# Performance work log

Measured on AMD Instinct MI355X. Metric: run time of the kernel, lower is better.

## Reference

```python
import jax, jax.numpy as jnp
import numpy as np

B, L, D, H, HID = 2048, 512, 17, 8, 256  # batch, max entities, feat dim, heads, mlp hidden
SPECIAL, OUT = 9, 23  # special vector dims, policy logits (7+16)


def _lin(k, out_d, in_d, scale):
    kw, kb = jax.random.split(k)
    W = jax.random.normal(kw, (out_d, in_d), jnp.float32) * scale
    b = jax.random.normal(kb, (out_d,), jnp.float32) * 0.01
    return W, b


def setup_inputs() -> dict:
    key = jax.random.key(0)
    ks = jax.random.split(key, 16)
    # observations: row 0 holds the 9-dim special vector, rows 1..L are ragged entities
    x = jax.random.normal(ks[0], (B, L + 1, D), jnp.float32)
    lengths = jax.random.randint(ks[1], (B,), 1, L + 1)
    mask = (jnp.arange(L)[None, :] < lengths[:, None]).astype(jnp.float32)
    x = x.at[:, 1:, :].multiply(mask[:, :, None])  # zero rows mark padding
    s = 1.0 / np.sqrt(D)
    # per-head K/V projections (num_heads separate tiny Linears)
    Wk = jax.random.normal(ks[2], (H, D, D), jnp.float32) * s
    bk = jax.random.normal(ks[3], (H, D), jnp.float32) * 0.01
    Wv = jax.random.normal(ks[4], (H, D, D), jnp.float32) * s
    bv = jax.random.normal(ks[5], (H, D), jnp.float32) * 0.01
    q = jax.random.normal(ks[6], (H, D), jnp.float32)  # learned per-head queries
    Wo, bo = _lin(ks[7], D, H * D, 1.0 / np.sqrt(H * D))
    sc = 1.0 / np.sqrt(D + SPECIAL)
    pW1, pb1 = _lin(ks[8], HID, D + SPECIAL, sc)
    pW2, pb2 = _lin(ks[9], HID, HID, 1.0 / np.sqrt(HID))
    pW3, pb3 = _lin(ks[10], OUT, HID, 1.0 / np.sqrt(HID))
    vW1, vb1 = _lin(ks[11], HID, D + SPECIAL, sc)
    vW2, vb2 = _lin(ks[12], HID, HID, 1.0 / np.sqrt(HID))
    vW3, vb3 = _lin(ks[13], 1, HID, 1.0 / np.sqrt(HID))
    return dict(x=x, Wk=Wk, bk=bk, Wv=Wv, bv=bv, q=q, Wo=Wo, bo=bo,
                pW1=pW1, pb1=pb1, pW2=pW2, pb2=pb2, pW3=pW3, pb3=pb3,
                vW1=vW1, vb1=vb1, vW2=vW2, vb2=vb2, vW3=vW3, vb3=vb3)


def _mlp(h, W1, b1, W2, b2, W3, b3):
    h = jax.nn.relu(h @ W1.T + b1)
    h = jax.nn.relu(h @ W2.T + b2)
    return h @ W3.T + b3


def reference(x, Wk, bk, Wv, bv, q, Wo, bo,
              pW1, pb1, pW2, pb2, pW3, pb3,
              vW1, vb1, vW2, vb2, vW3, vb3):
    special = x[:, 0, :SPECIAL]            # [B, 9]
    seq = x[:, 1:, :]                      # [B, L, D]
    mask = jnp.sum(jnp.abs(seq), axis=-1) != 0  # [B, L] non-padded rows
    # per-head keys/values for all samples at once (batched over the head loop)
    keys = jnp.einsum('bld,hed->bhle', seq, Wk) + bk[None, :, None, :]   # [B,H,L,D]
    vals = jnp.einsum('bld,hed->bhle', seq, Wv) + bv[None, :, None, :]   # [B,H,L,D]
    scores = jnp.einsum('bhle,he->bhl', keys, q)                          # [B,H,L]
    scores = jnp.where(mask[:, None, :], scores, -1e9)
    w = jax.nn.softmax(scores, axis=-1)                                   # [B,H,L]
    agg = jnp.einsum('bhl,bhle->bhe', w, vals).reshape(x.shape[0], H * D)  # concat heads
    attn = agg @ Wo.T + bo                                                # [B, D]
    comb = jnp.concatenate([attn, special], axis=-1)                      # [B, D+9]
    logits = _mlp(comb, pW1, pb1, pW2, pb2, pW3, pb3)                     # [B, 23]
    value = _mlp(comb, vW1, vb1, vW2, vb2, vW3, vb3)                      # [B, 1]
    return logits, value
```

## Files before the change

### kernel.cpp

```cpp
#include <hip/hip_runtime.h>
#include <hip/hip_bf16.h>

#define B_ 2048
#define D_ 17
#define H_ 8
#define HID_ 256
#define OUT_ 23
#define XROW 8721
#define SEQN 8704
#define ROWP 20
#define LAST4 4465151

__device__ __forceinline__ float bclane(float v, int l) {
  return __uint_as_float(__builtin_amdgcn_readlane(__float_as_uint(v), l));
}

__global__ __launch_bounds__(256) void prep_kernel(
    const float* __restrict__ pW2, const float* __restrict__ vW2,
    const float* __restrict__ Wk, const float* __restrict__ bk,
    const float* __restrict__ q,
    float* __restrict__ pW2t, float* __restrict__ vW2t, float* __restrict__ qkc)
{
  const int bid = blockIdx.x;
  const int t = threadIdx.x;
  if (bid == 128) {
    if (t < H_ * D_) {
      const int h = t / D_, dd = t - h * D_;
      float s = 0.f;
      #pragma unroll
      for (int e = 0; e < D_; ++e) s = fmaf(Wk[h*289 + e*D_ + dd], q[h*D_ + e], s);
      qkc[h*18 + dd] = s;
    } else if (t < H_ * D_ + H_) {
      const int h = t - H_ * D_;
      float s = 0.f;
      #pragma unroll
      for (int e = 0; e < D_; ++e) s = fmaf(bk[h*D_ + e], q[h*D_ + e], s);
      qkc[h*18 + 17] = s;
    }
    return;
  }
  __shared__ float tile[32][33];
  const int m = bid >> 6, tid = bid & 63;
  const int ti = (tid >> 3) * 32, tk = (tid & 7) * 32;
  const float* src = m ? vW2 : pW2;
  float* dst = m ? vW2t : pW2t;
  const int tx = t & 31, ty = t >> 5;
  #pragma unroll
  for (int r = 0; r < 4; ++r) tile[ty + 8*r][tx] = src[(ti + ty + 8*r)*HID_ + tk + tx];
  __syncthreads();
  #pragma unroll
  for (int r = 0; r < 4; ++r) dst[(tk + ty + 8*r)*HID_ + ti + tx] = tile[tx][ty + 8*r];
}

__device__ __forceinline__ void stw(float* s_seq, int off, float val) {
  if ((unsigned)off < (unsigned)SEQN) {
    const int r = off / 17;
    const int c = off - r * 17;
    s_seq[r * ROWP + c] = val;
  }
}
__device__ __forceinline__ void stw4(float* s_seq, int off, float4 v) {
  stw(s_seq, off,     v.x);
  stw(s_seq, off + 1, v.y);
  stw(s_seq, off + 2, v.z);
  stw(s_seq, off + 3, v.w);
}

__global__ __launch_bounds__(256, 3) void attn_comb_kernel(
    const float* __restrict__ x, const float* __restrict__ qkc,
    const float* __restrict__ Wv, const float* __restrict__ bv,
    const float* __restrict__ Wo, const float* __restrict__ bo,
    float* __restrict__ comb)
{
  __shared__ __align__(16) float s_seq[512 * ROWP];
  __shared__ float s_part[4][H_][18];
  __shared__ float s_swn[136];
  __shared__ float s_agg[136];
  __shared__ float s_wp[136];

  const int t = threadIdx.x;
  const int b = blockIdx.x;
  const int w = t >> 6, lane = t & 63;
  const int hp = lane >> 4;
  const int rg = lane & 15;
  const int seq0 = b * XROW + D_;
  const int s4 = seq0 >> 2;
  const int phase = seq0 & 3;
  const float4* __restrict__ x4 = (const float4*)x;

  const float pv = x[seq0 + lane * 136];

  float4 s0, s1, s2, s3, sR4, s5, s6, s7, s8;
  s0  = x4[s4 + t];
  s1  = x4[s4 +  256 + t];
  s2  = x4[s4 +  512 + t];
  s3  = x4[s4 +  768 + t];
  sR4 = x4[s4 + 1024 + t];

  const unsigned long long live = __ballot(pv != 0.f) | 1ull;
  const int nrows = 8 * (64 - __builtin_clzll(live));
  const int rounds = min(9, (nrows * D_ + phase + 1023) >> 10);

  if (rounds > 5) s5 = x4[s4 + 1280 + t];
  if (rounds > 6) s6 = x4[s4 + 1536 + t];
  if (rounds > 7) s7 = x4[s4 + 1792 + t];
  int idx8 = s4 + 2048 + t; if (idx8 > LAST4) idx8 = LAST4;
  if (rounds > 8) s8 = x4[idx8];

  const float* q0 = qkc + (2*hp) * 18;
  float qk0[D_], qk1[D_];
  #pragma unroll
  for (int d = 0; d < D_; ++d) { qk0[d] = q0[d]; qk1[d] = q0[18 + d]; }
  const float ch0 = q0[17], ch1 = q0[35];

  {
    const int o0 = 4*t - phase;
    stw4(s_seq, o0,        s0);
    stw4(s_seq, o0 + 1024, s1);
    stw4(s_seq, o0 + 2048, s2);
    stw4(s_seq, o0 + 3072, s3);
    stw4(s_seq, o0 + 4096, sR4);
    if (rounds > 5) stw4(s_seq, o0 + 5120, s5);
    if (rounds > 6) stw4(s_seq, o0 + 6144, s6);
    if (rounds > 7) stw4(s_seq, o0 + 7168, s7);
    if (rounds > 8) stw4(s_seq, 4*idx8 - seq0, s8);
  }
  __syncthreads();

  float den0 = 0.f, den1 = 0.f;
  float acc0[D_], acc1[D_];
  #pragma unroll
  for (int d = 0; d < D_; ++d) { acc0[d] = 0.f; acc1[d] = 0.f; }

  auto dorow = [&](int row) {
    const bool ok = row < nrows;
    const float* rp = &s_seq[(ok ? row : 0) * ROWP];
    const float4 v0 = *(const float4*)rp;
    const float4 v1 = *(const float4*)(rp + 4);
    const float4 v2 = *(const float4*)(rp + 8);
    const float4 v3 = *(const float4*)(rp + 12);
    const float4 v4 = *(const float4*)(rp + 16);
    float sA = ch0, sB = ch1;
    sA = fmaf(qk0[0],  v0.x, sA); sB = fmaf(qk1[0],  v0.x, sB);
    sA = fmaf(qk0[1],  v0.y, sA); sB = fmaf(qk1[1],  v0.y, sB);
    sA = fmaf(qk0[2],  v0.z, sA); sB = fmaf(qk1[2],  v0.z, sB);
    sA = fmaf(qk0[3],  v0.w, sA); sB = fmaf(qk1[3],  v0.w, sB);
    sA = fmaf(qk0[4],  v1.x, sA); sB = fmaf(qk1[4],  v1.x, sB);
    sA = fmaf(qk0[5],  v1.y, sA); sB = fmaf(qk1[5],  v1.y, sB);
    sA = fmaf(qk0[6],  v1.z, sA); sB = fmaf(qk1[6],  v1.z, sB);
    sA = fmaf(qk0[7],  v1.w, sA); sB = fmaf(qk1[7],  v1.w, sB);
    sA = fmaf(qk0[8],  v2.x, sA); sB = fmaf(qk1[8],  v2.x, sB);
    sA = fmaf(qk0[9],  v2.y, sA); sB = fmaf(qk1[9],  v2.y, sB);
    sA = fmaf(qk0[10], v2.z, sA); sB = fmaf(qk1[10], v2.z, sB);
    sA = fmaf(qk0[11], v2.w, sA); sB = fmaf(qk1[11], v2.w, sB);
    sA = fmaf(qk0[12], v3.x, sA); sB = fmaf(qk1[12], v3.x, sB);
    sA = fmaf(qk0[13], v3.y, sA); sB = fmaf(qk1[13], v3.y, sB);
    sA = fmaf(qk0[14], v3.z, sA); sB = fmaf(qk1[14], v3.z, sB);
    sA = fmaf(qk0[15], v3.w, sA); sB = fmaf(qk1[15], v3.w, sB);
    sA = fmaf(qk0[16], v4.x, sA); sB = fmaf(qk1[16], v4.x, sB);
    const bool lv = ok && (v0.x != 0.f);
    const float p0 = lv ? __expf(sA) : 0.f;
    const float p1 = lv ? __expf(sB) : 0.f;
    den0 += p0; den1 += p1;
    acc0[0]  = fmaf(p0, v0.x, acc0[0]);  acc1[0]  = fmaf(p1, v0.x, acc1[0]);
    acc0[1]  = fmaf(p0, v0.y, acc0[1]);  acc1[1]  = fmaf(p1, v0.y, acc1[1]);
    acc0[2]  = fmaf(p0, v0.z, acc0[2]);  acc1[2]  = fmaf(p1, v0.z, acc1[2]);
    acc0[3]  = fmaf(p0, v0.w, acc0[3]);  acc1[3]  = fmaf(p1, v0.w, acc1[3]);
    acc0[4]  = fmaf(p0, v1.x, acc0[4]);  acc1[4]  = fmaf(p1, v1.x, acc1[4]);
    acc0[5]  = fmaf(p0, v1.y, acc0[5]);  acc1[5]  = fmaf(p1, v1.y, acc1[5]);
    acc0[6]  = fmaf(p0, v1.z, acc0[6]);  acc1[6]  = fmaf(p1, v1.z, acc1[6]);
    acc0[7]  = fmaf(p0, v1.w, acc0[7]);  acc1[7]  = fmaf(p1, v1.w, acc1[7]);
    acc0[8]  = fmaf(p0, v2.x, acc0[8]);  acc1[8]  = fmaf(p1, v2.x, acc1[8]);
    acc0[9]  = fmaf(p0, v2.y, acc0[9]);  acc1[9]  = fmaf(p1, v2.y, acc1[9]);
    acc0[10] = fmaf(p0, v2.z, acc0[10]); acc1[10] = fmaf(p1, v2.z, acc1[10]);
    acc0[11] = fmaf(p0, v2.w, acc0[11]); acc1[11] = fmaf(p1, v2.w, acc1[11]);
    acc0[12] = fmaf(p0, v3.x, acc0[12]); acc1[12] = fmaf(p1, v3.x, acc1[12]);
    acc0[13] = fmaf(p0, v3.y, acc0[13]); acc1[13] = fmaf(p1, v3.y, acc1[13]);
    acc0[14] = fmaf(p0, v3.z, acc0[14]); acc1[14] = fmaf(p1, v3.z, acc1[14]);
    acc0[15] = fmaf(p0, v3.w, acc0[15]); acc1[15] = fmaf(p1, v3.w, acc1[15]);
    acc0[16] = fmaf(p0, v4.x, acc0[16]); acc1[16] = fmaf(p1, v4.x, acc1[16]);
  };

  {
    const int s0r = w * 64;
    if (s0r < nrows) {
      dorow(s0r + rg);
      dorow(s0r + rg + 16);
      dorow(s0r + rg + 32);
      dorow(s0r + rg + 48);
    }
    const int s1r = 256 + w * 64;
    if (s1r < nrows) {
      dorow(s1r + rg);
      dorow(s1r + rg + 16);
      dorow(s1r + rg + 32);
      dorow(s1r + rg + 48);
    }
  }

  #pragma unroll
  for (int m = 1; m <= 8; m <<= 1) {
    den0 += __shfl_xor(den0, m, 64);
    den1 += __shfl_xor(den1, m, 64);
    #pragma unroll
    for (int d = 0; d < D_; ++d) {
      acc0[d] += __shfl_xor(acc0[d], m, 64);
      acc1[d] += __shfl_xor(acc1[d], m, 64);
    }
  }
  if (rg == 0) {
    float* p0p = &s_part[w][2*hp][0];
    float* p1p = &s_part[w][2*hp + 1][0];
    p0p[0] = den0; p1p[0] = den1;
    #pragma unroll
    for (int d = 0; d < D_; ++d) { p0p[1 + d] = acc0[d]; p1p[1 + d] = acc1[d]; }
  }
  __syncthreads();

  if (t < 136) {
    const int hh = t / D_, d = t - hh * D_;
    float dn = 0.f, ac = 0.f;
    #pragma unroll
    for (int ww = 0; ww < 4; ++ww) { dn += s_part[ww][hh][0]; ac += s_part[ww][hh][1 + d]; }
    s_swn[t] = ac / dn;
  }
  __syncthreads();
  if (t < 136) {
    const int hh = t / D_, e = t - hh * D_;
    float s = bv[t];
    #pragma unroll
    for (int d = 0; d < D_; ++d) s = fmaf(Wv[hh*289 + e*D_ + d], s_swn[hh*D_ + d], s);
    s_agg[t] = s;
  }
  __syncthreads();
  if (t < 136) {
    const int o = t >> 3, pt = t & 7;
    float s = 0.f;
    #pragma unroll
    for (int j = 0; j < D_; ++j) s = fmaf(Wo[o*136 + pt*D_ + j], s_agg[pt*D_ + j], s);
    s_wp[t] = s;
  }
  __syncthreads();
  if (t < D_) {
    float s = bo[t];
    #pragma unroll
    for (int pt = 0; pt < 8; ++pt) s += s_wp[t*8 + pt];
    comb[b*26 + t] = s;
  } else if (t < 26) {
    comb[b*26 + t] = x[b * XROW + (t - D_)];
  }
}

__global__ __launch_bounds__(512) void mlp_kernel(
    const float* __restrict__ comb,
    const float* __restrict__ pW1, const float* __restrict__ pb1,
    const float* __restrict__ pW2t, const float* __restrict__ pb2,
    const float* __restrict__ pW3, const float* __restrict__ pb3,
    const float* __restrict__ vW1, const float* __restrict__ vb1,
    const float* __restrict__ vW2t, const float* __restrict__ vb2,
    const float* __restrict__ vW3, const float* __restrict__ vb3,
    float* __restrict__ out)
{
  __shared__ float s_comb[8][26];
  __shared__ __align__(16) float s_red[2][3][8][HID_];
  __shared__ __align__(16) float s_h2[2][8][HID_];

  const int t = threadIdx.x;
  const int b0 = blockIdx.x * 8;
  const int p = t >> 8;
  const int kq = (t >> 6) & 3;
  const int ln = t & 63;

  if (t < 208) { const int bb = t / 26, k = t - bb*26; s_comb[bb][k] = comb[(size_t)(b0 + bb)*26 + k]; }
  __syncthreads();

  const float* W1  = p ? vW1  : pW1;   const float* B1 = p ? vb1 : pb1;
  const float* W2t = p ? vW2t : pW2t;  const float* B2 = p ? vb2 : pb2;

  float h[8];
  {
    const int i = kq * 64 + ln;
    float a[8];
    #pragma unroll
    for (int bb = 0; bb < 8; ++bb) a[bb] = 0.f;
    const float* wr = W1 + i * 26;
    for (int k = 0; k < 26; ++k) {
      const float wk = wr[k];
      #pragma unroll
      for (int bb = 0; bb < 8; ++bb) a[bb] = fmaf(wk, s_comb[bb][k], a[bb]);
    }
    const float bias = B1[i];
    #pragma unroll
    for (int bb = 0; bb < 8; ++bb) h[bb] = fmaxf(a[bb] + bias, 0.f);
  }

  float4 acc[8];
  #pragma unroll
  for (int bb = 0; bb < 8; ++bb) acc[bb] = make_float4(0.f, 0.f, 0.f, 0.f);
  {
    const float* wbase = W2t + (size_t)(kq * 64) * HID_ + 4 * ln;
    #pragma unroll 8
    for (int jj = 0; jj < 64; ++jj) {
      const float4 wv = *(const float4*)(wbase + (size_t)jj * HID_);
      #pragma unroll
      for (int bb = 0; bb < 8; ++bb) {
        const float hv = bclane(h[bb], jj);
        acc[bb].x = fmaf(wv.x, hv, acc[bb].x);
        acc[bb].y = fmaf(wv.y, hv, acc[bb].y);
        acc[bb].z = fmaf(wv.z, hv, acc[bb].z);
        acc[bb].w = fmaf(wv.w, hv, acc[bb].w);
      }
    }
  }
  if (kq > 0) {
    #pragma unroll
    for (int bb = 0; bb < 8; ++bb) *(float4*)&s_red[p][kq - 1][bb][4 * ln] = acc[bb];
  }
  __syncthreads();
  if (kq == 0) {
    const float4 bias = *(const float4*)&B2[4 * ln];
    #pragma unroll
    for (int bb = 0; bb < 8; ++bb) {
      const float4 r0 = *(const float4*)&s_red[p][0][bb][4 * ln];
      const float4 r1 = *(const float4*)&s_red[p][1][bb][4 * ln];
      const float4 r2 = *(const float4*)&s_red[p][2][bb][4 * ln];
      float4 rr;
      rr.x = fmaxf(acc[bb].x + r0.x + r1.x + r2.x + bias.x, 0.f);
      rr.y = fmaxf(acc[bb].y + r0.y + r1.y + r2.y + bias.y, 0.f);
      rr.z = fmaxf(acc[bb].z + r0.z + r1.z + r2.z + bias.z, 0.f);
      rr.w = fmaxf(acc[bb].w + r0.w + r1.w + r2.w + bias.w, 0.f);
      *(float4*)&s_h2[p][bb][4 * ln] = rr;
    }
  }
  __syncthreads();

  if (t < 184) {
    const int bb = t / OUT_, o = t - bb * OUT_;
    const float4* w4 = (const float4*)(pW3 + o * HID_);
    const float4* h4 = (const float4*)&s_h2[0][bb][0];
    float s = pb3[o];
    for (int k = 0; k < 64; ++k) {
      const float4 wv = w4[k], hv = h4[k];
      s = fmaf(wv.x, hv.x, fmaf(wv.y, hv.y, fmaf(wv.z, hv.z, fmaf(wv.w, hv.w, s))));
    }
    out[(size_t)(b0 + bb) * OUT_ + o] = s;
  } else if (t >= 256 && t < 264) {
    const int bb = t - 256;
    const float4* w4 = (const float4*)vW3;
    const float4* h4 = (const float4*)&s_h2[1][bb][0];
    float s = vb3[0];
    for (int k = 0; k < 64; ++k) {
      const float4 wv = w4[k], hv = h4[k];
      s = fmaf(wv.x, hv.x, fmaf(wv.y, hv.y, fmaf(wv.z, hv.z, fmaf(wv.w, hv.w, s))));
    }
    out[(size_t)B_ * OUT_ + b0 + bb] = s;
  }
}

extern "C" void kernel_launch(void* const* d_in, const int* in_sizes, int n_in,
                              void* d_out, int out_size, void* d_ws, size_t ws_size,
                              hipStream_t stream) {
  (void)in_sizes; (void)n_in; (void)out_size; (void)ws_size;
  const float* x   = (const float*)d_in[0];
  const float* Wk  = (const float*)d_in[1];
  const float* bk  = (const float*)d_in[2];
  const float* Wv  = (const float*)d_in[3];
  const float* bv  = (const float*)d_in[4];
  const float* q   = (const float*)d_in[5];
  const float* Wo  = (const float*)d_in[6];
  const float* bo  = (const float*)d_in[7];
  const float* pW1 = (const float*)d_in[8];
  const float* pb1 = (const float*)d_in[9];
  const float* pW2 = (const float*)d_in[10];
  const float* pb2 = (const float*)d_in[11];
  const float* pW3 = (const float*)d_in[12];
  const float* pb3 = (const float*)d_in[13];
  const float* vW1 = (const float*)d_in[14];
  const float* vb1 = (const float*)d_in[15];
  const float* vW2 = (const float*)d_in[16];
  const float* vb2 = (const float*)d_in[17];
  const float* vW3 = (const float*)d_in[18];
  const float* vb3 = (const float*)d_in[19];
  float* out = (float*)d_out;

  float* pW2t = (float*)d_ws;
  float* vW2t = pW2t + (size_t)HID_ * HID_;
  float* qkc  = vW2t + (size_t)HID_ * HID_;
  float* comb = qkc + 160;

  prep_kernel<<<129, 256, 0, stream>>>(pW2, vW2, Wk, bk, q, pW2t, vW2t, qkc);
  attn_comb_kernel<<<B_, 256, 0, stream>>>(x, qkc, Wv, bv, Wo, bo, comb);
  mlp_kernel<<<B_ / 8, 512, 0, stream>>>(comb, pW1, pb1, pW2t, pb2, pW3, pb3,
                                         vW1, vb1, vW2t, vb2, vW3, vb3, out);
}
```

Measured before the change: 56.67 us.

## Stage sequence tile via direct global-to-LDS loads with packed row layout

Replaces the register-staged float4 loads and the scalar divide-by-17 scatter into padded shared-memory rows with direct global_load_lds transfers that copy the raw contiguous sequence into LDS. Rows are then read at a stride of 17 floats offset by the alignment phase, using scalar LDS reads instead of float4 reads. This removes the integer division and scatter stores and frees registers, and the launch bound occupancy hint rises from 3 to 4 blocks. In exchange, the odd-stride scalar LDS reads may cause more bank traffic and more LDS instructions per row.

```diff
diff --git a/kernel.cpp b/kernel.cpp
--- a/kernel.cpp
+++ b/kernel.cpp
@@ -8,11 +8,19 @@
 #define OUT_ 23
 #define XROW 8721
 #define SEQN 8704
-#define ROWP 20
 #define LAST4 4465151
+
+typedef unsigned int u32;
+typedef const __attribute__((address_space(1))) u32* gp1_t;
+typedef __attribute__((address_space(3))) u32* lp3_t;
 
 __device__ __forceinline__ float bclane(float v, int l) {
   return __uint_as_float(__builtin_amdgcn_readlane(__float_as_uint(v), l));
+}
+
+__device__ __forceinline__ void gload_lds16(const float4* gsrc_lane, float* lds_wave_base) {
+  __builtin_amdgcn_global_load_lds((gp1_t)(const void*)gsrc_lane,
+                                   (lp3_t)(void*)lds_wave_base, 16, 0, 0);
 }
 
 __global__ __launch_bounds__(256) void prep_kernel(
@@ -52,27 +60,13 @@
   for (int r = 0; r < 4; ++r) dst[(tk + ty + 8*r)*HID_ + ti + tx] = tile[tx][ty + 8*r];
 }
 
-__device__ __forceinline__ void stw(float* s_seq, int off, float val) {
-  if ((unsigned)off < (unsigned)SEQN) {
-    const int r = off / 17;
-    const int c = off - r * 17;
-    s_seq[r * ROWP + c] = val;
-  }
-}
-__device__ __forceinline__ void stw4(float* s_seq, int off, float4 v) {
-  stw(s_seq, off,     v.x);
-  stw(s_seq, off + 1, v.y);
-  stw(s_seq, off + 2, v.z);
-  stw(s_seq, off + 3, v.w);
-}
-
-__global__ __launch_bounds__(256, 3) void attn_comb_kernel(
+__global__ __launch_bounds__(256, 4) void attn_comb_kernel(
     const float* __restrict__ x, const float* __restrict__ qkc,
     const float* __restrict__ Wv, const float* __restrict__ bv,
     const float* __restrict__ Wo, const float* __restrict__ bo,
     float* __restrict__ comb)
 {
-  __shared__ __align__(16) float s_seq[512 * ROWP];
+  __shared__ __align__(16) float s_seq[9216];
   __shared__ float s_part[4][H_][18];
   __shared__ float s_swn[136];
   __shared__ float s_agg[136];
@@ -90,22 +84,26 @@
 
   const float pv = x[seq0 + lane * 136];
 
-  float4 s0, s1, s2, s3, sR4, s5, s6, s7, s8;
-  s0  = x4[s4 + t];
-  s1  = x4[s4 +  256 + t];
-  s2  = x4[s4 +  512 + t];
-  s3  = x4[s4 +  768 + t];
-  sR4 = x4[s4 + 1024 + t];
-
-  const unsigned long long live = __ballot(pv != 0.f) | 1ull;
-  const int nrows = 8 * (64 - __builtin_clzll(live));
-  const int rounds = min(9, (nrows * D_ + phase + 1023) >> 10);
-
-  if (rounds > 5) s5 = x4[s4 + 1280 + t];
-  if (rounds > 6) s6 = x4[s4 + 1536 + t];
-  if (rounds > 7) s7 = x4[s4 + 1792 + t];
-  int idx8 = s4 + 2048 + t; if (idx8 > LAST4) idx8 = LAST4;
-  if (rounds > 8) s8 = x4[idx8];
+  {
+    float* dstb = s_seq + ((t & ~63) << 2);
+    const int g0 = s4 + t;
+    gload_lds16(x4 + g0,          dstb);
+    gload_lds16(x4 + g0 + 256,    dstb + 1024);
+    gload_lds16(x4 + g0 + 512,    dstb + 2048);
+    gload_lds16(x4 + g0 + 768,    dstb + 3072);
+    gload_lds16(x4 + g0 + 1024,   dstb + 4096);
+
+    const unsigned long long live = __ballot(pv != 0.f) | 1ull;
+    const int nr = 8 * (64 - __builtin_clzll(live));
+    const int rounds = min(9, (nr * D_ + phase + 1023) >> 10);
+
+    if (rounds > 5) gload_lds16(x4 + g0 + 1280, dstb + 5120);
+    if (rounds > 6) gload_lds16(x4 + g0 + 1536, dstb + 6144);
+    if (rounds > 7) gload_lds16(x4 + g0 + 1792, dstb + 7168);
+    if (rounds > 8) gload_lds16(x4 + min(g0 + 2048, LAST4), dstb + 8192);
+  }
+  const unsigned long long live2 = __ballot(pv != 0.f) | 1ull;
+  const int nrows = 8 * (64 - __builtin_clzll(live2));
 
   const float* q0 = qkc + (2*hp) * 18;
   float qk0[D_], qk1[D_];
@@ -113,18 +111,6 @@
   for (int d = 0; d < D_; ++d) { qk0[d] = q0[d]; qk1[d] = q0[18 + d]; }
   const float ch0 = q0[17], ch1 = q0[35];
 
-  {
-    const int o0 = 4*t - phase;
-    stw4(s_seq, o0,        s0);
-    stw4(s_seq, o0 + 1024, s1);
-    stw4(s_seq, o0 + 2048, s2);
-    stw4(s_seq, o0 + 3072, s3);
-    stw4(s_seq, o0 + 4096, sR4);
-    if (rounds > 5) stw4(s_seq, o0 + 5120, s5);
-    if (rounds > 6) stw4(s_seq, o0 + 6144, s6);
-    if (rounds > 7) stw4(s_seq, o0 + 7168, s7);
-    if (rounds > 8) stw4(s_seq, 4*idx8 - seq0, s8);
-  }
   __syncthreads();
 
   float den0 = 0.f, den1 = 0.f;
@@ -133,52 +119,51 @@
   for (int d = 0; d < D_; ++d) { acc0[d] = 0.f; acc1[d] = 0.f; }
 
   auto dorow = [&](int row) {
-    const bool ok = row < nrows;
-    const float* rp = &s_seq[(ok ? row : 0) * ROWP];
-    const float4 v0 = *(const float4*)rp;
-    const float4 v1 = *(const float4*)(rp + 4);
-    const float4 v2 = *(const float4*)(rp + 8);
-    const float4 v3 = *(const float4*)(rp + 12);
-    const float4 v4 = *(const float4*)(rp + 16);
+    const float* rp = &s_seq[phase + row * D_];
+    const float f0 = rp[0],  f1 = rp[1],  f2 = rp[2],  f3 = rp[3];
+    const float f4 = rp[4],  f5 = rp[5],  f6 = rp[6],  f7 = rp[7];
+    const float f8 = rp[8],  f9 = rp[9],  f10 = rp[10], f11 = rp[11];
+    const float f12 = rp[12], f13 = rp[13], f14 = rp[14], f15 = rp[15];
+    const float f16 = rp[16];
     float sA = ch0, sB = ch1;
-    sA = fmaf(qk0[0],  v0.x, sA); sB = fmaf(qk1[0],  v0.x, sB);
-    sA = fmaf(qk0[1],  v0.y, sA); sB = fmaf(qk1[1],  v0.y, sB);
-    sA = fmaf(qk0[2],  v0.z, sA); sB = fmaf(qk1[2],  v0.z, sB);
-    sA = fmaf(qk0[3],  v0.w, sA); sB = fmaf(qk1[3],  v0.w, sB);
-    sA = fmaf(qk0[4],  v1.x, sA); sB = fmaf(qk1[4],  v1.x, sB);
-    sA = fmaf(qk0[5],  v1.y, sA); sB = fmaf(qk1[5],  v1.y, sB);
-    sA = fmaf(qk0[6],  v1.z, sA); sB = fmaf(qk1[6],  v1.z, sB);
-    sA = fmaf(qk0[7],  v1.w, sA); sB = fmaf(qk1[7],  v1.w, sB);
-    sA = fmaf(qk0[8],  v2.x, sA); sB = fmaf(qk1[8],  v2.x, sB);
-    sA = fmaf(qk0[9],  v2.y, sA); sB = fmaf(qk1[9],  v2.y, sB);
-    sA = fmaf(qk0[10], v2.z, sA); sB = fmaf(qk1[10], v2.z, sB);
-    sA = fmaf(qk0[11], v2.w, sA); sB = fmaf(qk1[11], v2.w, sB);
-    sA = fmaf(qk0[12], v3.x, sA); sB = fmaf(qk1[12], v3.x, sB);
-    sA = fmaf(qk0[13], v3.y, sA); sB = fmaf(qk1[13], v3.y, sB);
-    sA = fmaf(qk0[14], v3.z, sA); sB = fmaf(qk1[14], v3.z, sB);
-    sA = fmaf(qk0[15], v3.w, sA); sB = fmaf(qk1[15], v3.w, sB);
-    sA = fmaf(qk0[16], v4.x, sA); sB = fmaf(qk1[16], v4.x, sB);
-    const bool lv = ok && (v0.x != 0.f);
+    sA = fmaf(qk0[0],  f0,  sA); sB = fmaf(qk1[0],  f0,  sB);
+    sA = fmaf(qk0[1],  f1,  sA); sB = fmaf(qk1[1],  f1,  sB);
+    sA = fmaf(qk0[2],  f2,  sA); sB = fmaf(qk1[2],  f2,  sB);
+    sA = fmaf(qk0[3],  f3,  sA); sB = fmaf(qk1[3],  f3,  sB);
+    sA = fmaf(qk0[4],  f4,  sA); sB = fmaf(qk1[4],  f4,  sB);
+    sA = fmaf(qk0[5],  f5,  sA); sB = fmaf(qk1[5],  f5,  sB);
+    sA = fmaf(qk0[6],  f6,  sA); sB = fmaf(qk1[6],  f6,  sB);
+    sA = fmaf(qk0[7],  f7,  sA); sB = fmaf(qk1[7],  f7,  sB);
+    sA = fmaf(qk0[8],  f8,  sA); sB = fmaf(qk1[8],  f8,  sB);
+    sA = fmaf(qk0[9],  f9,  sA); sB = fmaf(qk1[9],  f9,  sB);
+    sA = fmaf(qk0[10], f10, sA); sB = fmaf(qk1[10], f10, sB);
+    sA = fmaf(qk0[11], f11, sA); sB = fmaf(qk1[11], f11, sB);
+    sA = fmaf(qk0[12], f12, sA); sB = fmaf(qk1[12], f12, sB);
+    sA = fmaf(qk0[13], f13, sA); sB = fmaf(qk1[13], f13, sB);
+    sA = fmaf(qk0[14], f14, sA); sB = fmaf(qk1[14], f14, sB);
+    sA = fmaf(qk0[15], f15, sA); sB = fmaf(qk1[15], f15, sB);
+    sA = fmaf(qk0[16], f16, sA); sB = fmaf(qk1[16], f16, sB);
+    const bool lv = (row < nrows) && (f0 != 0.f);
     const float p0 = lv ? __expf(sA) : 0.f;
     const float p1 = lv ? __expf(sB) : 0.f;
     den0 += p0; den1 += p1;
-    acc0[0]  = fmaf(p0, v0.x, acc0[0]);  acc1[0]  = fmaf(p1, v0.x, acc1[0]);
-    acc0[1]  = fmaf(p0, v0.y, acc0[1]);  acc1[1]  = fmaf(p1, v0.y, acc1[1]);
-    acc0[2]  = fmaf(p0, v0.z, acc0[2]);  acc1[2]  = fmaf(p1, v0.z, acc1[2]);
-    acc0[3]  = fmaf(p0, v0.w, acc0[3]);  acc1[3]  = fmaf(p1, v0.w, acc1[3]);
-    acc0[4]  = fmaf(p0, v1.x, acc0[4]);  acc1[4]  = fmaf(p1, v1.x, acc1[4]);
-    acc0[5]  = fmaf(p0, v1.y, acc0[5]);  acc1[5]  = fmaf(p1, v1.y, acc1[5]);
-    acc0[6]  = fmaf(p0, v1.z, acc0[6]);  acc1[6]  = fmaf(p1, v1.z, acc1[6]);
-    acc0[7]  = fmaf(p0, v1.w, acc0[7]);  acc1[7]  = fmaf(p1, v1.w, acc1[7]);
-    acc0[8]  = fmaf(p0, v2.x, acc0[8]);  acc1[8]  = fmaf(p1, v2.x, acc1[8]);
-    acc0[9]  = fmaf(p0, v2.y, acc0[9]);  acc1[9]  = fmaf(p1, v2.y, acc1[9]);
-    acc0[10] = fmaf(p0, v2.z, acc0[10]); acc1[10] = fmaf(p1, v2.z, acc1[10]);
-    acc0[11] = fmaf(p0, v2.w, acc0[11]); acc1[11] = fmaf(p1, v2.w, acc1[11]);
-    acc0[12] = fmaf(p0, v3.x, acc0[12]); acc1[12] = fmaf(p1, v3.x, acc1[12]);
-    acc0[13] = fmaf(p0, v3.y, acc0[13]); acc1[13] = fmaf(p1, v3.y, acc1[13]);
-    acc0[14] = fmaf(p0, v3.z, acc0[14]); acc1[14] = fmaf(p1, v3.z, acc1[14]);
-    acc0[15] = fmaf(p0, v3.w, acc0[15]); acc1[15] = fmaf(p1, v3.w, acc1[15]);
-    acc0[16] = fmaf(p0, v4.x, acc0[16]); acc1[16] = fmaf(p1, v4.x, acc1[16]);
+    acc0[0]  = fmaf(p0, f0,  acc0[0]);  acc1[0]  = fmaf(p1, f0,  acc1[0]);
+    acc0[1]  = fmaf(p0, f1,  acc0[1]);  acc1[1]  = fmaf(p1, f1,  acc1[1]);
+    acc0[2]  = fmaf(p0, f2,  acc0[2]);  acc1[2]  = fmaf(p1, f2,  acc1[2]);
+    acc0[3]  = fmaf(p0, f3,  acc0[3]);  acc1[3]  = fmaf(p1, f3,  acc1[3]);
+    acc0[4]  = fmaf(p0, f4,  acc0[4]);  acc1[4]  = fmaf(p1, f4,  acc1[4]);
+    acc0[5]  = fmaf(p0, f5,  acc0[5]);  acc1[5]  = fmaf(p1, f5,  acc1[5]);
+    acc0[6]  = fmaf(p0, f6,  acc0[6]);  acc1[6]  = fmaf(p1, f6,  acc1[6]);
+    acc0[7]  = fmaf(p0, f7,  acc0[7]);  acc1[7]  = fmaf(p1, f7,  acc1[7]);
+    acc0[8]  = fmaf(p0, f8,  acc0[8]);  acc1[8]  = fmaf(p1, f8,  acc1[8]);
+    acc0[9]  = fmaf(p0, f9,  acc0[9]);  acc1[9]  = fmaf(p1, f9,  acc1[9]);
+    acc0[10] = fmaf(p0, f10, acc0[10]); acc1[10] = fmaf(p1, f10, acc1[10]);
+    acc0[11] = fmaf(p0, f11, acc0[11]); acc1[11] = fmaf(p1, f11, acc1[11]);
+    acc0[12] = fmaf(p0, f12, acc0[12]); acc1[12] = fmaf(p1, f12, acc1[12]);
+    acc0[13] = fmaf(p0, f13, acc0[13]); acc1[13] = fmaf(p1, f13, acc1[13]);
+    acc0[14] = fmaf(p0, f14, acc0[14]); acc1[14] = fmaf(p1, f14, acc1[14]);
+    acc0[15] = fmaf(p0, f15, acc0[15]); acc1[15] = fmaf(p1, f15, acc1[15]);
+    acc0[16] = fmaf(p0, f16, acc0[16]); acc1[16] = fmaf(p1, f16, acc1[16]);
   };
 
   {
```

Measured after the change: 52.72 us, median of 2. 1.07x faster.
